# Kernel tuning notes

Measured on AMD Instinct MI355X. Metric: run time of the kernel, lower is better.

Reference implementation:

```python
import jax, jax.numpy as jnp
import numpy as np

N, E, R, H = 20000, 320000, 8, 4
KG, CC = 128, 4
IN, HID, OUT = 256, 256, 256  # in_channels = KG + 128 (GCN out)
HO1, HO2 = HID // H, OUT // H  # per-head out channels
SLOPE_ACT = 0.01   # nn.LeakyReLU default
SLOPE_ATT = 0.2    # RGATConv negative_slope default


def gcn_conv(x, W, b, src, dst):
    """PyG GCNConv: add self loops, symmetric norm, x@W, scatter-sum, +bias."""
    n = x.shape[0]
    loop = jnp.arange(n, dtype=src.dtype)
    s = jnp.concatenate([src, loop])
    d = jnp.concatenate([dst, loop])
    deg = jnp.zeros((n,), x.dtype).at[d].add(1.0)
    dis = jnp.where(deg > 0, jax.lax.rsqrt(jnp.maximum(deg, 1.0)), 0.0)
    norm = dis[s] * dis[d]                        # [E+N]
    h = x @ W                                     # [n, out]
    out = jax.ops.segment_sum(norm[:, None] * h[s], d, num_segments=n)
    return out + b


def rgat_conv(x, W, q, k, b, src, dst, edge_type, heads, oc):
    """PyG RGATConv (additive-self-attention, across-relation, dim=1, concat)."""
    n = x.shape[0]
    xw = jnp.einsum('ni,rio->rno', x, W)          # [R, n, heads*oc]
    out_i = xw[edge_type, dst]                    # [E, heads*oc]
    out_j = xw[edge_type, src]                    # [E, heads*oc]
    qi = out_i @ q                                # [E, heads]
    kj = out_j @ k                                # [E, heads]
    alpha = jax.nn.leaky_relu(qi + kj, SLOPE_ATT)
    # softmax over incoming edges per destination node (across-relation)
    amax = jax.ops.segment_max(alpha, dst, num_segments=n)[dst]
    ex = jnp.exp(alpha - amax)
    denom = jax.ops.segment_sum(ex, dst, num_segments=n)[dst]
    alpha = ex / denom                            # [E, heads]
    e = src.shape[0]
    msg = (alpha[:, :, None] * out_j.reshape(e, heads, oc)).reshape(e, heads * oc)
    out = jax.ops.segment_sum(msg, dst, num_segments=n) + b
    return out, alpha


def setup_inputs() -> dict:
    key = jax.random.key(0)
    ks = jax.random.split(key, 16)
    d = {}
    d['kg_emb'] = jax.random.normal(ks[0], (N, KG), jnp.float32)
    d['ccle0'] = jax.random.normal(ks[1], (N, CC), jnp.float32)
    d['gcn_w1'] = jax.random.normal(ks[2], (CC, 32), jnp.float32) / np.float32(np.sqrt(CC))
    d['gcn_b1'] = jnp.zeros((32,), jnp.float32)
    d['gcn_w2'] = jax.random.normal(ks[3], (32, 128), jnp.float32) / np.float32(np.sqrt(32))
    d['gcn_b2'] = jnp.zeros((128,), jnp.float32)
    d['rgat1_w'] = jax.random.normal(ks[4], (R, IN, HID), jnp.float32) / np.float32(np.sqrt(IN))
    d['rgat1_q'] = jax.random.normal(ks[5], (HID, H), jnp.float32) / np.float32(np.sqrt(HID))
    d['rgat1_k'] = jax.random.normal(ks[6], (HID, H), jnp.float32) / np.float32(np.sqrt(HID))
    d['rgat1_b'] = jnp.zeros((HID,), jnp.float32)
    d['rgat2_w'] = jax.random.normal(ks[7], (R, HID, OUT), jnp.float32) / np.float32(np.sqrt(HID))
    d['rgat2_q'] = jax.random.normal(ks[8], (OUT, H), jnp.float32) / np.float32(np.sqrt(OUT))
    d['rgat2_k'] = jax.random.normal(ks[9], (OUT, H), jnp.float32) / np.float32(np.sqrt(OUT))
    d['rgat2_b'] = jnp.zeros((OUT,), jnp.float32)
    d['lin_w'] = jax.random.normal(ks[10], (IN, OUT), jnp.float32) / np.float32(np.sqrt(IN))
    d['lin_b'] = jnp.zeros((OUT,), jnp.float32)
    d['edge_index'] = jax.random.randint(ks[11], (2, E), 0, N, jnp.int32)
    d['edge_type'] = jax.random.randint(ks[12], (E,), 0, R, jnp.int32)
    return d


def reference(kg_emb, ccle0, gcn_w1, gcn_b1, gcn_w2, gcn_b2,
              rgat1_w, rgat1_q, rgat1_k, rgat1_b,
              rgat2_w, rgat2_q, rgat2_k, rgat2_b,
              lin_w, lin_b, edge_index, edge_type):
    src, dst = edge_index[0], edge_index[1]
    # ccle_layer: GCN(4->32) -> LeakyReLU -> GCN(32->128)
    c = gcn_conv(ccle0, gcn_w1, gcn_b1, src, dst)
    c = jax.nn.leaky_relu(c, SLOPE_ACT)
    c = gcn_conv(c, gcn_w2, gcn_b2, src, dst)
    # node_id = arange(N): concat(kg_emb, ccle_out)
    x0 = jnp.concatenate([kg_emb, c], axis=1)     # [N, IN]
    h, a1 = rgat_conv(x0, rgat1_w, rgat1_q, rgat1_k, rgat1_b,
                      src, dst, edge_type, H, HO1)
    h = jax.nn.leaky_relu(h, SLOPE_ACT)           # dropout p=0 -> identity
    h, a2 = rgat_conv(h, rgat2_w, rgat2_q, rgat2_k, rgat2_b,
                      src, dst, edge_type, H, HO2)
    out = h + (x0 @ lin_w + lin_b)                # residual through self.lin
    return out, a1, a2
```

## Files before the change

kernel.cpp:

```cpp
#include <hip/hip_runtime.h>
#include <cstdint>

static constexpr int N = 20000;
static constexpr int E = 320000;
static constexpr int R = 8;
static constexpr int H = 4;
static constexpr int C = 256;

using short8 = __attribute__((ext_vector_type(8))) short;
using f32x4  = __attribute__((ext_vector_type(4))) float;

__device__ __forceinline__ float lrelu(float x, float s) { return x >= 0.f ? x : s * x; }
__device__ __forceinline__ unsigned short f2bf(float f) {
    unsigned u = __float_as_uint(f);
    unsigned r = (u + 0x7FFFu + ((u >> 16) & 1u)) >> 16;
    return (unsigned short)r;
}
__device__ __forceinline__ float bf2f(unsigned short s) {
    return __uint_as_float(((unsigned)s) << 16);
}

__device__ __forceinline__ void gl2l16(const unsigned short* g, unsigned short* l) {
    __builtin_amdgcn_global_load_lds(
        (const __attribute__((address_space(1))) unsigned int*)g,
        (__attribute__((address_space(3))) unsigned int*)l, 16, 0, 0);
}

__global__ void k_zero_int(int* p, int n) {
    int i = blockIdx.x * blockDim.x + threadIdx.x;
    if (i < n) p[i] = 0;
}

__global__ void k_count(const int* __restrict__ ei, int* __restrict__ cnt) {
    int e = blockIdx.x * blockDim.x + threadIdx.x;
    if (e < E) atomicAdd(&cnt[ei[E + e]], 1);
}

__global__ __launch_bounds__(1024) void k_scan(const int* __restrict__ cnt,
                                               int* __restrict__ rowptr,
                                               int* __restrict__ cursor,
                                               float* __restrict__ dis) {
    __shared__ int part[1024];
    const int CH = (N + 1023) / 1024;
    int t = threadIdx.x;
    int base = t * CH;
    int sum = 0;
    for (int j = 0; j < CH; ++j) {
        int idx = base + j;
        if (idx < N) sum += cnt[idx];
    }
    part[t] = sum;
    __syncthreads();
    for (int off = 1; off < 1024; off <<= 1) {
        int v = 0;
        if (t >= off) v = part[t - off];
        __syncthreads();
        if (t >= off) part[t] += v;
        __syncthreads();
    }
    int run = part[t] - sum;
    for (int j = 0; j < CH; ++j) {
        int idx = base + j;
        if (idx < N) {
            int cv = cnt[idx];
            rowptr[idx] = run;
            cursor[idx] = run;
            dis[idx] = rsqrtf((float)cv + 1.0f);
            run += cv;
        }
    }
    if (t == 1023) rowptr[N] = part[1023];
}

__global__ void k_scatter(const int* __restrict__ ei, const int* __restrict__ et,
                          int* __restrict__ cursor, int* __restrict__ csr_se,
                          int* __restrict__ csr_eid) {
    int e = blockIdx.x * blockDim.x + threadIdx.x;
    if (e >= E) return;
    int d = ei[E + e];
    int pos = atomicAdd(&cursor[d], 1);
    csr_se[pos] = (et[e] << 16) | ei[e];
    csr_eid[pos] = e;
}

__global__ void k_h1(const float* __restrict__ x, const float* __restrict__ W,
                     float* __restrict__ h) {
    int idx = blockIdx.x * blockDim.x + threadIdx.x;
    if (idx >= N * 32) return;
    int n = idx >> 5, f = idx & 31;
    const float* xr = x + n * 4;
    float acc = 0.f;
#pragma unroll
    for (int c = 0; c < 4; ++c) acc += xr[c] * W[c * 32 + f];
    h[idx] = acc;
}

__global__ void k_agg32(const int* __restrict__ rowptr, const int* __restrict__ csr_se,
                        const float* __restrict__ dis, const float* __restrict__ h,
                        const float* __restrict__ b, float* __restrict__ c) {
    int idx = blockIdx.x * blockDim.x + threadIdx.x;
    if (idx >= N * 32) return;
    int d = idx >> 5, f = idx & 31;
    int beg = rowptr[d], end = rowptr[d + 1];
    float acc = 0.f;
    for (int i = beg; i < end; ++i) {
        int s = csr_se[i] & 0xFFFF;
        acc += dis[s] * h[s * 32 + f];
    }
    float dd = dis[d];
    c[idx] = dd * acc + dd * dd * h[idx] + b[f];
}

__global__ void k_h2kg(const float* __restrict__ c1, const float* __restrict__ W,
                       const float* __restrict__ kg, unsigned short* __restrict__ h,
                       float* __restrict__ x0, unsigned short* __restrict__ xb0) {
    int idx = blockIdx.x * blockDim.x + threadIdx.x;
    if (idx >= N * 128) return;
    int n = idx >> 7, f = idx & 127;
    const float* cr = c1 + n * 32;
    float acc = 0.f;
    for (int c = 0; c < 32; ++c) acc += lrelu(cr[c], 0.01f) * W[c * 128 + f];
    h[idx] = f2bf(acc);
    float v = kg[idx];
    x0[n * 256 + f] = v;
    xb0[n * 256 + f] = f2bf(v);
}

__global__ void k_agg128(const int* __restrict__ rowptr, const int* __restrict__ csr_se,
                         const float* __restrict__ dis,
                         const unsigned short* __restrict__ h,
                         const float* __restrict__ b, float* __restrict__ x0,
                         unsigned short* __restrict__ xb0) {
    int idx = blockIdx.x * blockDim.x + threadIdx.x;
    if (idx >= N * 128) return;
    int d = idx >> 7, f = idx & 127;
    int beg = rowptr[d], end = rowptr[d + 1];
    float acc = 0.f;
    int i = beg;
    for (; i + 2 <= end; i += 2) {
        int s0 = csr_se[i] & 0xFFFF;
        int s1 = csr_se[i + 1] & 0xFFFF;
        float d0 = dis[s0], d1 = dis[s1];
        float v0 = bf2f(h[s0 * 128 + f]), v1 = bf2f(h[s1 * 128 + f]);
        acc += d0 * v0 + d1 * v1;
    }
    if (i < end) {
        int s = csr_se[i] & 0xFFFF;
        acc += dis[s] * bf2f(h[s * 128 + f]);
    }
    float dd = dis[d];
    float v = dd * acc + dd * dd * bf2f(h[d * 128 + f]) + b[f];
    x0[d * 256 + 128 + f] = v;
    xb0[d * 256 + 128 + f] = f2bf(v);
}

__global__ __launch_bounds__(256) void k_wqkb(const float* __restrict__ W,
                                              const float* __restrict__ q,
                                              const float* __restrict__ kmat,
                                              unsigned short* __restrict__ wqkb) {
    int w = (blockIdx.x * blockDim.x + threadIdx.x) >> 6;
    int lane = threadIdx.x & 63;
    int r = w >> 8, i = w & 255;
    const float* wr = W + ((size_t)(r * 256 + i)) * 256;
    float4 a = *(const float4*)(wr + lane * 4);
    float aq0 = 0.f, aq1 = 0.f, aq2 = 0.f, aq3 = 0.f;
    float ak0 = 0.f, ak1 = 0.f, ak2 = 0.f, ak3 = 0.f;
    int o = lane * 4;
    const float av[4] = {a.x, a.y, a.z, a.w};
#pragma unroll
    for (int j = 0; j < 4; ++j) {
        float4 qv = *(const float4*)(q + (o + j) * 4);
        float4 kv = *(const float4*)(kmat + (o + j) * 4);
        aq0 += av[j] * qv.x; aq1 += av[j] * qv.y;
        aq2 += av[j] * qv.z; aq3 += av[j] * qv.w;
        ak0 += av[j] * kv.x; ak1 += av[j] * kv.y;
        ak2 += av[j] * kv.z; ak3 += av[j] * kv.w;
    }
#pragma unroll
    for (int d = 1; d < 64; d <<= 1) {
        aq0 += __shfl_xor(aq0, d); aq1 += __shfl_xor(aq1, d);
        aq2 += __shfl_xor(aq2, d); aq3 += __shfl_xor(aq3, d);
        ak0 += __shfl_xor(ak0, d); ak1 += __shfl_xor(ak1, d);
        ak2 += __shfl_xor(ak2, d); ak3 += __shfl_xor(ak3, d);
    }
    if (lane == 0) {
        int nq = r * 4, nk = 32 + r * 4;
        wqkb[(nq + 0) * 256 + i] = f2bf(aq0);
        wqkb[(nq + 1) * 256 + i] = f2bf(aq1);
        wqkb[(nq + 2) * 256 + i] = f2bf(aq2);
        wqkb[(nq + 3) * 256 + i] = f2bf(aq3);
        wqkb[(nk + 0) * 256 + i] = f2bf(ak0);
        wqkb[(nk + 1) * 256 + i] = f2bf(ak1);
        wqkb[(nk + 2) * 256 + i] = f2bf(ak2);
        wqkb[(nk + 3) * 256 + i] = f2bf(ak3);
    }
}

#define QP 264
__global__ __launch_bounds__(256) void k_qnkn_mfma(
    const unsigned short* __restrict__ xb, const unsigned short* __restrict__ wqkb,
    float* __restrict__ qn, float* __restrict__ kn)
{
    __shared__ unsigned short Ws[64 * QP];
    int t = threadIdx.x;
    {
        int r = t >> 2, off = (t & 3) * 64;
#pragma unroll
        for (int i = 0; i < 8; ++i)
            *(uint4*)(&Ws[r * QP + off + i * 8]) =
                *(const uint4*)(wqkb + r * 256 + off + i * 8);
    }
    __syncthreads();
    int wave = t >> 6, lane = t & 63;
    int lrow = lane & 15, kq = lane >> 4;
    int mw = blockIdx.x * 64 + wave * 16;
    int gm = mw + lrow;
    int gmc = gm < N ? gm : N - 1;

    f32x4 acc[4];
#pragma unroll
    for (int j = 0; j < 4; ++j) acc[j] = (f32x4){0.f, 0.f, 0.f, 0.f};

    for (int k0 = 0; k0 < 8; ++k0) {
        short8 af = *(const short8*)(xb + (size_t)gmc * 256 + k0 * 32 + kq * 8);
#pragma unroll
        for (int j = 0; j < 4; ++j) {
            short8 bf4 = *(const short8*)(&Ws[(j * 16 + lrow) * QP + k0 * 32 + kq * 8]);
            acc[j] = __builtin_amdgcn_mfma_f32_16x16x32_bf16(af, bf4, acc[j], 0, 0, 0);
        }
    }
#pragma unroll
    for (int j = 0; j < 4; ++j) {
        int col = j * 16 + lrow;
#pragma unroll
        for (int reg = 0; reg < 4; ++reg) {
            int gr = mw + kq * 4 + reg;
            if (gr < N) {
                if (col < 32) qn[gr * 32 + col] = acc[j][reg];
                else          kn[gr * 32 + (col - 32)] = acc[j][reg];
            }
        }
    }
}

__global__ void k_soft(const int* __restrict__ rowptr, const int* __restrict__ csr_se,
                       const int* __restrict__ csr_eid,
                       const float* __restrict__ qn, const float* __restrict__ kn,
                       float* __restrict__ alpha_csr, float* __restrict__ aout) {
    int wid = (blockIdx.x * blockDim.x + threadIdx.x) >> 6;
    int lane = threadIdx.x & 63;
    if (wid >= N) return;
    int d = wid;
    int beg = rowptr[d], end = rowptr[d + 1];
    if (beg >= end) return;
    int slot = lane >> 2, h = lane & 3;
    int nc = (end - beg + 15) >> 4;
    const float* qrow = qn + d * 32;

    auto rawv = [&](int i) {
        int se = csr_se[i];
        int tt = se >> 16, s = se & 0xFFFF;
        return lrelu(qrow[tt * 4 + h] + kn[s * 32 + tt * 4 + h], 0.2f);
    };

    float av[4];
    float m = -1e30f;
    for (int c = 0; c < nc; ++c) {
        int i = beg + c * 16 + slot;
        float v = (i < end) ? rawv(i) : -1e30f;
        if (c < 4) av[c] = v;
        m = fmaxf(m, v);
    }
    m = fmaxf(m, __shfl_xor(m, 4));
    m = fmaxf(m, __shfl_xor(m, 8));
    m = fmaxf(m, __shfl_xor(m, 16));
    m = fmaxf(m, __shfl_xor(m, 32));

    float sum = 0.f;
    for (int c = 0; c < nc; ++c) {
        int i = beg + c * 16 + slot;
        float ex = 0.f;
        if (i < end) {
            float v = (c < 4) ? av[c] : rawv(i);
            ex = expf(v - m);
        }
        if (c < 4) av[c] = ex;
        sum += ex;
    }
    sum += __shfl_xor(sum, 4);
    sum += __shfl_xor(sum, 8);
    sum += __shfl_xor(sum, 16);
    sum += __shfl_xor(sum, 32);
    float inv = 1.f / sum;

    for (int c = 0; c < nc; ++c) {
        int i = beg + c * 16 + slot;
        if (i < end) {
            float ex = (c < 4) ? av[c] : expf(rawv(i) - m);
            float a = ex * inv;
            alpha_csr[i * 4 + h] = a;
            aout[csr_eid[i] * 4 + h] = a;
        }
    }
}

#define WTP 72
__global__ __launch_bounds__(256) void k_wconv_t(const float* __restrict__ W,
                                                 unsigned short* __restrict__ Wt) {
    int bid = blockIdx.x;
    int z = bid >> 4;
    int tile = bid & 15;
    int k0 = (tile >> 2) * 64, n0 = (tile & 3) * 64;
    __shared__ unsigned short T[64 * WTP];
    int t = threadIdx.x;
    const float* Wz = W + ((size_t)z << 16);
    int r = t >> 4;
    int cs = (t & 15) * 4;
#pragma unroll
    for (int rr = 0; rr < 4; ++rr) {
        int k = r + rr * 16;
        float4 v = *(const float4*)(Wz + (size_t)(k0 + k) * 256 + n0 + cs);
        T[(cs + 0) * WTP + k] = f2bf(v.x);
        T[(cs + 1) * WTP + k] = f2bf(v.y);
        T[(cs + 2) * WTP + k] = f2bf(v.z);
        T[(cs + 3) * WTP + k] = f2bf(v.w);
    }
    __syncthreads();
    int n = t >> 2, ck = (t & 3) * 16;
    unsigned short* dst = Wt + ((size_t)z << 16) + (size_t)(n0 + n) * 256 + k0 + ck;
    const unsigned short* srcp = T + n * WTP + ck;
    *(uint4*)(dst) = *(const uint4*)(srcp);
    *(uint4*)(dst + 8) = *(const uint4*)(srcp + 8);
}

#define TM 128
#define TN 128
__global__ __launch_bounds__(256) void gemm_mfma4(
    const unsigned short* __restrict__ A, const unsigned short* __restrict__ Bt,
    unsigned short* __restrict__ Cbf, float* __restrict__ Cf,
    const float* __restrict__ bias, const float* __restrict__ bias2,
    int M, int NZ, int NT, int MT, int zlin)
{
    __shared__ unsigned short As[128 * 32];
    __shared__ unsigned short Bs[128 * 32];

    int bi = blockIdx.x;
    int cx = bi & 7;
    int g = bi >> 3;
    int per = NZ * NT;
    int mh = g / per;
    int j  = g % per;
    int mt = mh * 8 + cx;
    if (mt >= MT) return;
    int z  = j % NZ;
    int nb = j / NZ;
    int m0 = mt * TM;
    int n0 = nb * TN;

    const unsigned short* Bz = Bt + ((size_t)z << 16);
    int t = threadIdx.x;
    int wave = t >> 6, lane = t & 63;
    int wr = wave >> 1, wc = wave & 1;
    int lrow = lane & 15, kq = lane >> 4;

    int sr0 = (wave * 2 + 0) * 16 + (lane >> 2);
    int sr1 = (wave * 2 + 1) * 16 + (lane >> 2);
    int sc = (lane & 3) * 8;
    int gm0 = m0 + sr0; if (gm0 >= M) gm0 = M - 1;
    int gm1 = m0 + sr1; if (gm1 >= M) gm1 = M - 1;
    const unsigned short* gA0 = A + (size_t)gm0 * 256 + sc;
    const unsigned short* gA1 = A + (size_t)gm1 * 256 + sc;
    const unsigned short* gB0 = Bz + (size_t)(n0 + sr0) * 256 + sc;
    const unsigned short* gB1 = Bz + (size_t)(n0 + sr1) * 256 + sc;
    unsigned short* lA0 = &As[(wave * 2 + 0) * 512];
    unsigned short* lA1 = &As[(wave * 2 + 1) * 512];
    unsigned short* lB0 = &Bs[(wave * 2 + 0) * 512];
    unsigned short* lB1 = &Bs[(wave * 2 + 1) * 512];

    f32x4 acc[4][4];
#pragma unroll
    for (int i = 0; i < 4; ++i)
#pragma unroll
        for (int jj = 0; jj < 4; ++jj) acc[i][jj] = (f32x4){0.f, 0.f, 0.f, 0.f};

    for (int k0 = 0; k0 < 256; k0 += 32) {
        gl2l16(gA0 + k0, lA0);
        gl2l16(gA1 + k0, lA1);
        gl2l16(gB0 + k0, lB0);
        gl2l16(gB1 + k0, lB1);
        __syncthreads();
        short8 af[4], bf4[4];
#pragma unroll
        for (int i = 0; i < 4; ++i)
            af[i] = *(const short8*)(&As[(wr * 64 + i * 16 + lrow) * 32 + kq * 8]);
#pragma unroll
        for (int jj = 0; jj < 4; ++jj)
            bf4[jj] = *(const short8*)(&Bs[(wc * 64 + jj * 16 + lrow) * 32 + kq * 8]);
#pragma unroll
        for (int i = 0; i < 4; ++i)
#pragma unroll
            for (int jj = 0; jj < 4; ++jj)
                acc[i][jj] = __builtin_amdgcn_mfma_f32_16x16x32_bf16(af[i], bf4[jj],
                                                                     acc[i][jj], 0, 0, 0);
        __syncthreads();
    }
    if (z == zlin) {
#pragma unroll
        for (int i = 0; i < 4; ++i)
#pragma unroll
            for (int jj = 0; jj < 4; ++jj) {
                int gn = n0 + wc * 64 + jj * 16 + lrow;
                float bsum = bias[gn] + bias2[gn];
#pragma unroll
                for (int reg = 0; reg < 4; ++reg) {
                    int gm = m0 + wr * 64 + i * 16 + kq * 4 + reg;
                    if (gm < M) Cf[(size_t)gm * 256 + gn] = acc[i][jj][reg] + bsum;
                }
            }
    } else {
#pragma unroll
        for (int i = 0; i < 4; ++i)
#pragma unroll
            for (int jj = 0; jj < 4; ++jj) {
                int gn = n0 + wc * 64 + jj * 16 + lrow;
#pragma unroll
                for (int reg = 0; reg < 4; ++reg) {
                    int gm = m0 + wr * 64 + i * 16 + kq * 4 + reg;
                    if (gm < M)
                        Cbf[((size_t)z * M + gm) * 256 + gn] = f2bf(acc[i][jj][reg]);
                }
            }
    }
}

__global__ __launch_bounds__(256) void k_msg_gather(
    const int* __restrict__ rowptr, const int* __restrict__ csr_se,
    const float* __restrict__ alpha_csr, const unsigned short* __restrict__ xw,
    const float* __restrict__ bias, float* __restrict__ out,
    unsigned short* __restrict__ xbout, int r0, int r1, int first, int act) {
    __shared__ float Pf[2][256];
    int tid = threadIdx.x;
    int wave = tid >> 6, lane = tid & 63;
    int nslot = wave >> 1, p = wave & 1;
    int node = blockIdx.x * 2 + nslot;
    int hsel = lane >> 4;
    float ax = 0.f, ay = 0.f, az = 0.f, aw = 0.f;

    auto edge = [&](int i) {
        int se = csr_se[i];
        int tt = se >> 16;
        if (tt >= r0 && tt < r1) {
            int s = se & 0xFFFF;
            float a = alpha_csr[i * 4 + hsel];
            uint2 pv = *(const uint2*)(xw + ((size_t)(tt - r0) * N + s) * 256 + lane * 4);
            ax += a * __uint_as_float(pv.x << 16);
            ay += a * __uint_as_float(pv.x & 0xFFFF0000u);
            az += a * __uint_as_float(pv.y << 16);
            aw += a * __uint_as_float(pv.y & 0xFFFF0000u);
        }
    };

    if (node < N) {
        int beg = rowptr[node], end = rowptr[node + 1];
        int i = beg + p;
        for (; i + 2 < end; i += 4) { edge(i); edge(i + 2); }
        if (i < end) edge(i);
    }
    if (p == 1) {
        float4 v = {ax, ay, az, aw};
        *(float4*)(&Pf[nslot][lane * 4]) = v;
    }
    __syncthreads();
    if (p == 0 && node < N) {
        float4 q = *(const float4*)(&Pf[nslot][lane * 4]);
        ax += q.x; ay += q.y; az += q.z; aw += q.w;
        float* o = out + (size_t)node * 256 + lane * 4;
        float vx, vy, vz, vw;
        if (first) {
            const float4 b = ((const float4*)bias)[lane];
            vx = ax + b.x; vy = ay + b.y; vz = az + b.z; vw = aw + b.w;
        } else {
            vx = o[0] + ax; vy = o[1] + ay; vz = o[2] + az; vw = o[3] + aw;
        }
        if (act) {
            vx = lrelu(vx, 0.01f); vy = lrelu(vy, 0.01f);
            vz = lrelu(vz, 0.01f); vw = lrelu(vw, 0.01f);
            unsigned short* xo = xbout + (size_t)node * 256 + lane * 4;
            xo[0] = f2bf(vx); xo[1] = f2bf(vy); xo[2] = f2bf(vz); xo[3] = f2bf(vw);
        }
        o[0] = vx; o[1] = vy; o[2] = vz; o[3] = vw;
    }
}

extern "C" void kernel_launch(void* const* d_in, const int* in_sizes, int n_in,
                              void* d_out, int out_size, void* d_ws, size_t ws_size,
                              hipStream_t stream) {
    const float* kg   = (const float*)d_in[0];
    const float* cc0  = (const float*)d_in[1];
    const float* gw1  = (const float*)d_in[2];
    const float* gb1  = (const float*)d_in[3];
    const float* gw2  = (const float*)d_in[4];
    const float* gb2  = (const float*)d_in[5];
    const float* r1w  = (const float*)d_in[6];
    const float* r1q  = (const float*)d_in[7];
    const float* r1k  = (const float*)d_in[8];
    const float* r1b  = (const float*)d_in[9];
    const float* r2w  = (const float*)d_in[10];
    const float* r2q  = (const float*)d_in[11];
    const float* r2k  = (const float*)d_in[12];
    const float* r2b  = (const float*)d_in[13];
    const float* linw = (const float*)d_in[14];
    const float* linb = (const float*)d_in[15];
    const int*   ei   = (const int*)d_in[16];
    const int*   et   = (const int*)d_in[17];

    float* out = (float*)d_out;
    float* a1  = out + (size_t)N * C;
    float* a2  = a1 + (size_t)E * H;

    float* ws = (float*)d_ws;
    size_t off = 0;
    float* dis  = ws + off; off += N;
    float* h1   = ws + off; off += (size_t)N * 32;
    float* c1   = ws + off; off += (size_t)N * 32;
    unsigned short* h2b = (unsigned short*)(ws + off); off += (size_t)N * 64;
    float* x0   = ws + off; off += (size_t)N * C;
    float* hmid = ws + off; off += (size_t)N * C;
    float* qn   = ws + off; off += (size_t)N * R * H;
    float* kn   = ws + off; off += (size_t)N * R * H;
    int* cnt     = (int*)(ws + off); off += N;
    int* rowptr  = (int*)(ws + off); off += N + 1;
    int* cursor  = (int*)(ws + off); off += N;
    int* csr_se  = (int*)(ws + off); off += E;
    int* csr_eid = (int*)(ws + off); off += E;
    float* alpha = ws + off; off += (size_t)E * H;
    unsigned short* xb0 = (unsigned short*)(ws + off); off += (size_t)N * 128;
    unsigned short* xb1 = (unsigned short*)(ws + off); off += (size_t)N * 128;
    unsigned short* wt  = (unsigned short*)(ws + off); off += (size_t)(R + 1) * 32768;
    unsigned short* wtl = wt + ((size_t)R << 16);
    unsigned short* wqkb = (unsigned short*)(ws + off); off += 8192;
    unsigned short* xwb = (unsigned short*)(ws + off);

    size_t fixedB = off * 4;
    int K = R;
    if (ws_size > fixedB) {
        size_t kmax = (ws_size - fixedB) / ((size_t)N * C * 2);
        if (kmax < (size_t)K) K = (int)kmax;
    } else {
        K = 1;
    }
    if (K < 1) K = 1;

    const int B = 256;
    auto cdiv = [](long a, long b) { return (int)((a + b - 1) / b); };
    const int MT = cdiv(N, TM);
    const int NT = C / TN;

    k_zero_int<<<cdiv(N, B), B, 0, stream>>>(cnt, N);
    k_count<<<cdiv(E, B), B, 0, stream>>>(ei, cnt);
    k_scan<<<1, 1024, 0, stream>>>(cnt, rowptr, cursor, dis);
    k_scatter<<<cdiv(E, B), B, 0, stream>>>(ei, et, cursor, csr_se, csr_eid);

    k_h1<<<cdiv((long)N * 32, B), B, 0, stream>>>(cc0, gw1, h1);
    k_agg32<<<cdiv((long)N * 32, B), B, 0, stream>>>(rowptr, csr_se, dis, h1, gb1, c1);
    k_h2kg<<<cdiv((long)N * 128, B), B, 0, stream>>>(c1, gw2, kg, h2b, x0, xb0);
    k_agg128<<<cdiv((long)N * 128, B), B, 0, stream>>>(rowptr, csr_se, dis, h2b,
                                                       gb2, x0, xb0);

    auto rgat = [&](unsigned short* xb, const float* W,
                    const float* q, const float* kk, const float* b,
                    float* obuf, unsigned short* xbout, float* aout,
                    int first, int act, int lin, float* linout,
                    const float* lb1, const float* lb2) {
        k_wqkb<<<512, 256, 0, stream>>>(W, q, kk, wqkb);
        k_qnkn_mfma<<<cdiv(N, 64), B, 0, stream>>>(xb, wqkb, qn, kn);
        k_soft<<<cdiv((long)N * 64, B), B, 0, stream>>>(rowptr, csr_se, csr_eid,
                                                        qn, kn, alpha, aout);
        k_wconv_t<<<R * 16, 256, 0, stream>>>(W, wt);
        for (int r0 = 0; r0 < R; r0 += K) {
            int kc = (R - r0) < K ? (R - r0) : K;
            int addlin = (lin && (r0 + kc == R)) ? 1 : 0;
            int nz = kc + addlin;
            int zl = addlin ? kc : -1;
            int gx = 8 * nz * NT * cdiv(MT, 8);
            gemm_mfma4<<<gx, 256, 0, stream>>>(xb, wt + ((size_t)r0 << 16), xwb,
                                               linout, lb1, lb2,
                                               N, nz, NT, MT, zl);
            int last = (r0 + kc >= R) ? 1 : 0;
            k_msg_gather<<<cdiv(N, 2), 256, 0, stream>>>(
                rowptr, csr_se, alpha, xwb, b, obuf, xbout, r0, r0 + kc,
                (first && r0 == 0) ? 1 : 0, act && last);
        }
    };

    k_wconv_t<<<16, 256, 0, stream>>>(linw, wtl);

    rgat(xb0, r1w, r1q, r1k, r1b, hmid, xb1, a1, 1, 1,
         1, out, linb, r2b);

    rgat(xb1, r2w, r2q, r2k, r2b, out, nullptr, a2, 0, 0,
         0, nullptr, nullptr, nullptr);
}
```

Measured before the change: 518.2 us.

## Double-buffer GEMM LDS tiles and XOR-swizzle columns to avoid bank conflicts

```diff
diff --git a/kernel.cpp b/kernel.cpp
--- a/kernel.cpp
+++ b/kernel.cpp
@@ -341,8 +341,8 @@
     const float* __restrict__ bias, const float* __restrict__ bias2,
     int M, int NZ, int NT, int MT, int zlin)
 {
-    __shared__ unsigned short As[128 * 32];
-    __shared__ unsigned short Bs[128 * 32];
+    __shared__ unsigned short As[2][128 * 32];
+    __shared__ unsigned short Bs[2][128 * 32];
 
     int bi = blockIdx.x;
     int cx = bi & 7;
@@ -365,17 +365,22 @@
 
     int sr0 = (wave * 2 + 0) * 16 + (lane >> 2);
     int sr1 = (wave * 2 + 1) * 16 + (lane >> 2);
-    int sc = (lane & 3) * 8;
+    int sc = (((lane & 3) ^ ((lane >> 3) & 3))) * 8;
     int gm0 = m0 + sr0; if (gm0 >= M) gm0 = M - 1;
     int gm1 = m0 + sr1; if (gm1 >= M) gm1 = M - 1;
     const unsigned short* gA0 = A + (size_t)gm0 * 256 + sc;
     const unsigned short* gA1 = A + (size_t)gm1 * 256 + sc;
     const unsigned short* gB0 = Bz + (size_t)(n0 + sr0) * 256 + sc;
     const unsigned short* gB1 = Bz + (size_t)(n0 + sr1) * 256 + sc;
-    unsigned short* lA0 = &As[(wave * 2 + 0) * 512];
-    unsigned short* lA1 = &As[(wave * 2 + 1) * 512];
-    unsigned short* lB0 = &Bs[(wave * 2 + 0) * 512];
-    unsigned short* lB1 = &Bs[(wave * 2 + 1) * 512];
+
+    auto stage = [&](int b, int ko) {
+        gl2l16(gA0 + ko, &As[b][(wave * 2 + 0) * 512]);
+        gl2l16(gA1 + ko, &As[b][(wave * 2 + 1) * 512]);
+        gl2l16(gB0 + ko, &Bs[b][(wave * 2 + 0) * 512]);
+        gl2l16(gB1 + ko, &Bs[b][(wave * 2 + 1) * 512]);
+    };
+
+    int rg = (kq ^ ((lrow >> 1) & 3)) * 8;
 
     f32x4 acc[4][4];
 #pragma unroll
@@ -383,19 +388,20 @@
 #pragma unroll
         for (int jj = 0; jj < 4; ++jj) acc[i][jj] = (f32x4){0.f, 0.f, 0.f, 0.f};
 
-    for (int k0 = 0; k0 < 256; k0 += 32) {
-        gl2l16(gA0 + k0, lA0);
-        gl2l16(gA1 + k0, lA1);
-        gl2l16(gB0 + k0, lB0);
-        gl2l16(gB1 + k0, lB1);
-        __syncthreads();
+    stage(0, 0);
+    __syncthreads();
+
+    int cur = 0;
+#pragma unroll 1
+    for (int step = 0; step < 8; ++step) {
+        if (step < 7) stage(cur ^ 1, (step + 1) * 32);
         short8 af[4], bf4[4];
 #pragma unroll
         for (int i = 0; i < 4; ++i)
-            af[i] = *(const short8*)(&As[(wr * 64 + i * 16 + lrow) * 32 + kq * 8]);
+            af[i] = *(const short8*)(&As[cur][(wr * 64 + i * 16 + lrow) * 32 + rg]);
 #pragma unroll
         for (int jj = 0; jj < 4; ++jj)
-            bf4[jj] = *(const short8*)(&Bs[(wc * 64 + jj * 16 + lrow) * 32 + kq * 8]);
+            bf4[jj] = *(const short8*)(&Bs[cur][(wc * 64 + jj * 16 + lrow) * 32 + rg]);
 #pragma unroll
         for (int i = 0; i < 4; ++i)
 #pragma unroll
@@ -403,6 +409,7 @@
                 acc[i][jj] = __builtin_amdgcn_mfma_f32_16x16x32_bf16(af[i], bf4[jj],
                                                                      acc[i][jj], 0, 0, 0);
         __syncthreads();
+        cur ^= 1;
     }
     if (z == zlin) {
 #pragma unroll
```

Result: slower. 529.1 us (+2.1%).
